# Kernel optimization log

Hardware: AMD Instinct MI355X
Metric: run time of the kernel (lower is better)

Reference implementation:

```python
import jax, jax.numpy as jnp
import numpy as np

N = 50000
NEG_SLOPE = 0.2
BN_EPS = 1e-5


def _self_loops(src, dst, n):
    loop = jnp.arange(n, dtype=src.dtype)
    return jnp.concatenate([src, loop]), jnp.concatenate([dst, loop])


def gcn_conv(x, src, dst, W, b, n):
    # PyG GCNConv: add self-loops, symmetric deg^-1/2 normalization, scatter-add.
    h = x @ W                                             # [N, C]
    s, d = _self_loops(src, dst, n)
    deg = jax.ops.segment_sum(jnp.ones_like(d, dtype=h.dtype), d, num_segments=n)
    dinv = jnp.where(deg > 0, jax.lax.rsqrt(deg), 0.0)
    norm = dinv[s] * dinv[d]                              # [E+N]
    out = jax.ops.segment_sum(h[s] * norm[:, None], d, num_segments=n)
    return out + b


def gat_conv(x, src, dst, W, a_src, a_dst, b, n, heads):
    # PyG GATConv (concat=False, eval mode: no dropout): add self-loops,
    # per-edge LeakyReLU attention logits, segment-softmax over dst, mean heads.
    C = W.shape[1] // heads
    h = (x @ W).reshape(n, heads, C)                      # [N, H, C]
    s, d = _self_loops(src, dst, n)
    al_s = jnp.sum(h * a_src[None], axis=-1)              # [N, H]
    al_d = jnp.sum(h * a_dst[None], axis=-1)              # [N, H]
    e = jax.nn.leaky_relu(al_s[s] + al_d[d], NEG_SLOPE)   # [E+N, H]
    emax = jax.ops.segment_max(e, d, num_segments=n)[d]
    ex = jnp.exp(e - emax)
    denom = jax.ops.segment_sum(ex, d, num_segments=n)[d]
    alpha = ex / denom                                    # [E+N, H]
    out = jax.ops.segment_sum(h[s] * alpha[:, :, None], d, num_segments=n)
    return jnp.mean(out, axis=1) + b                      # concat=False -> head mean


def batch_norm(x, g, b, m, v):
    # eval-mode BatchNorm1d with running stats
    return (x - m) * jax.lax.rsqrt(v + BN_EPS) * g + b


def setup_inputs() -> dict:
    key = jax.random.key(0)
    ks = jax.random.split(key, 12)
    E = 800000
    inp = {}
    inp['x'] = jax.random.normal(ks[0], (N, 128), dtype=jnp.float32)
    inp['edge_index'] = jax.random.randint(ks[1], (2, E), 0, N, dtype=jnp.int64)
    inp['gcn1_W'] = jax.random.normal(ks[2], (128, 96), dtype=jnp.float32) * 0.08
    inp['gcn1_b'] = jnp.zeros((96,), jnp.float32)
    inp['bn1_g'] = jnp.ones((96,), jnp.float32)
    inp['bn1_b'] = jnp.zeros((96,), jnp.float32)
    inp['bn1_m'] = jnp.zeros((96,), jnp.float32)
    inp['bn1_v'] = jnp.ones((96,), jnp.float32)
    inp['gat1_W'] = jax.random.normal(ks[3], (96, 192), dtype=jnp.float32) * 0.1
    inp['gat1_as'] = jax.random.normal(ks[4], (2, 96), dtype=jnp.float32) * 0.1
    inp['gat1_ad'] = jax.random.normal(ks[5], (2, 96), dtype=jnp.float32) * 0.1
    inp['gat1_b'] = jnp.zeros((96,), jnp.float32)
    inp['gcn2_W'] = jax.random.normal(ks[6], (96, 96), dtype=jnp.float32) * 0.1
    inp['gcn2_b'] = jnp.zeros((96,), jnp.float32)
    inp['bn2_g'] = jnp.ones((96,), jnp.float32)
    inp['bn2_b'] = jnp.zeros((96,), jnp.float32)
    inp['bn2_m'] = jnp.zeros((96,), jnp.float32)
    inp['bn2_v'] = jnp.ones((96,), jnp.float32)
    inp['gat2_W'] = jax.random.normal(ks[7], (96, 80), dtype=jnp.float32) * 0.1
    inp['gat2_as'] = jax.random.normal(ks[8], (2, 40), dtype=jnp.float32) * 0.1
    inp['gat2_ad'] = jax.random.normal(ks[9], (2, 40), dtype=jnp.float32) * 0.1
    inp['gat2_b'] = jnp.zeros((40,), jnp.float32)
    return inp


def reference(x, edge_index, gcn1_W, gcn1_b, bn1_g, bn1_b, bn1_m, bn1_v,
              gat1_W, gat1_as, gat1_ad, gat1_b, gcn2_W, gcn2_b,
              bn2_g, bn2_b, bn2_m, bn2_v, gat2_W, gat2_as, gat2_ad, gat2_b):
    src, dst = edge_index[0], edge_index[1]
    h = gcn_conv(x, src, dst, gcn1_W, gcn1_b, N)
    h = jax.nn.relu(batch_norm(h, bn1_g, bn1_b, bn1_m, bn1_v))
    h = jax.nn.relu(gat_conv(h, src, dst, gat1_W, gat1_as, gat1_ad, gat1_b, N, 2))
    h = gcn_conv(h, src, dst, gcn2_W, gcn2_b, N)
    h = jax.nn.relu(batch_norm(h, bn2_g, bn2_b, bn2_m, bn2_v))
    h = gat_conv(h, src, dst, gat2_W, gat2_as, gat2_ad, gat2_b, N, 2)
    return jax.nn.log_softmax(h, axis=1)
```

## Files before the change

### kernel.cpp

```cpp
#include <hip/hip_runtime.h>
#include <math.h>

#define NNODES 50000
#define NEG_SLOPE 0.2f
#define BN_EPS 1e-5f

typedef __attribute__((ext_vector_type(8))) short bf16x8;
typedef __attribute__((ext_vector_type(4))) float f32x4;

static __device__ __forceinline__ float leaky(float x) {
    return x > 0.f ? x : NEG_SLOPE * x;
}
static __device__ __forceinline__ unsigned short f2bf(float x) {
    unsigned u = __float_as_uint(x);
    u += 0x7FFFu + ((u >> 16) & 1u);
    return (unsigned short)(u >> 16);
}
static __device__ __forceinline__ void unpack8(uint4 u, float* v) {
    v[0] = __uint_as_float(u.x << 16);
    v[1] = __uint_as_float(u.x & 0xFFFF0000u);
    v[2] = __uint_as_float(u.y << 16);
    v[3] = __uint_as_float(u.y & 0xFFFF0000u);
    v[4] = __uint_as_float(u.z << 16);
    v[5] = __uint_as_float(u.z & 0xFFFF0000u);
    v[6] = __uint_as_float(u.w << 16);
    v[7] = __uint_as_float(u.w & 0xFFFF0000u);
}
static __device__ __forceinline__ void acc8(uint4 u, float w, float* a) {
    float v[8]; unpack8(u, v);
#pragma unroll
    for (int j = 0; j < 8; ++j) a[j] = fmaf(w, v[j], a[j]);
}
static __device__ __forceinline__ void add8(uint4 u, float* a) {
    float v[8]; unpack8(u, v);
#pragma unroll
    for (int j = 0; j < 8; ++j) a[j] += v[j];
}
static __device__ __forceinline__ uint4 pack8(const float* o) {
    uint4 r;
    r.x = ((unsigned)f2bf(o[1]) << 16) | f2bf(o[0]);
    r.y = ((unsigned)f2bf(o[3]) << 16) | f2bf(o[2]);
    r.z = ((unsigned)f2bf(o[5]) << 16) | f2bf(o[4]);
    r.w = ((unsigned)f2bf(o[7]) << 16) | f2bf(o[6]);
    return r;
}

__global__ void k_count(const int* __restrict__ dst, int* degi, int E) {
    int e = blockIdx.x * blockDim.x + threadIdx.x;
    if (e < E) atomicAdd(&degi[dst[e]], 1);
}
__global__ void k_scan1(const int* __restrict__ degi, int* __restrict__ incl,
                        int* __restrict__ bsum, int n) {
    __shared__ int s[256];
    int i = blockIdx.x * 256 + threadIdx.x;
    int v = (i < n) ? degi[i] : 0;
    s[threadIdx.x] = v;
    __syncthreads();
    for (int off = 1; off < 256; off <<= 1) {
        int t = (threadIdx.x >= (unsigned)off) ? s[threadIdx.x - off] : 0;
        __syncthreads();
        s[threadIdx.x] += t;
        __syncthreads();
    }
    if (i < n) incl[i] = s[threadIdx.x];
    if (threadIdx.x == 255) bsum[blockIdx.x] = s[255];
}
__global__ void k_scan2(int* bsum, int nb) {
    __shared__ int s[256];
    int v = ((int)threadIdx.x < nb) ? bsum[threadIdx.x] : 0;
    s[threadIdx.x] = v;
    __syncthreads();
    for (int off = 1; off < 256; off <<= 1) {
        int t = (threadIdx.x >= (unsigned)off) ? s[threadIdx.x - off] : 0;
        __syncthreads();
        s[threadIdx.x] += t;
        __syncthreads();
    }
    if ((int)threadIdx.x < nb) bsum[threadIdx.x] = s[threadIdx.x];
}
__global__ void k_scan3(const int* __restrict__ degi, const int* __restrict__ incl,
                        const int* __restrict__ bsum, int* __restrict__ row_ptr,
                        int* __restrict__ cursor, float* __restrict__ dinv, int n) {
    int i = blockIdx.x * 256 + threadIdx.x;
    if (i >= n) return;
    int off = (blockIdx.x > 0) ? bsum[blockIdx.x - 1] : 0;
    int inc = incl[i] + off;
    row_ptr[i + 1] = inc;
    cursor[i] = inc - degi[i];
    dinv[i] = rsqrtf((float)(degi[i] + 1));
    if (i == 0) row_ptr[0] = 0;
}
__global__ void k_fill(const int* __restrict__ src, const int* __restrict__ dst,
                       int* cursor, int* __restrict__ csr_src, int E) {
    int e = blockIdx.x * blockDim.x + threadIdx.x;
    if (e >= E) return;
    int pos = atomicAdd(&cursor[dst[e]], 1);
    csr_src[pos] = src[e];
}

__global__ void k_convall(const float4* __restrict__ x, uint4* __restrict__ xout,
                          const float* __restrict__ W1, unsigned short* __restrict__ w1T,
                          const float* __restrict__ W2, unsigned short* __restrict__ w2T,
                          const float* __restrict__ W3, unsigned short* __restrict__ w3T,
                          const float* __restrict__ W4, unsigned short* __restrict__ w4T,
                          int nx) {
    int i = blockIdx.x * blockDim.x + threadIdx.x;
    if (i < nx) {
        float4 a = x[i * 2], b = x[i * 2 + 1];
        float o[8] = {a.x, a.y, a.z, a.w, b.x, b.y, b.z, b.w};
        xout[i] = pack8(o);
        return;
    }
    int j = i - nx;
    if (j < 12288) {
        int k = j / 96, c = j % 96;
        w1T[c * 128 + k] = f2bf(W1[j]);
    } else if ((j -= 12288) < 18432) {
        int k = j / 192, c = j % 192;
        w2T[c * 96 + k] = f2bf(W2[j]);
    } else if ((j -= 18432) < 9216) {
        int k = j / 96, c = j % 96;
        w3T[c * 96 + k] = f2bf(W3[j]);
    } else if ((j -= 9216) < 7680) {
        int k = j / 80, c = j % 80;
        w4T[c * 96 + k] = f2bf(W4[j]);
    }
}

template<int KI, int KO, int HC, int SCALE>
__launch_bounds__(256)
__global__ void k_gemm_mfma(const unsigned short* __restrict__ A,
                            const unsigned short* __restrict__ WT,
                            unsigned short* __restrict__ C, int n,
                            const float* __restrict__ as, const float* __restrict__ ad,
                            float* __restrict__ alS, float* __restrict__ alD,
                            const float* __restrict__ dinv) {
    constexpr int KP = KI + 8;
    constexpr int NT = KO / 16;
    constexpr int KT = KI / 32;
    __shared__ unsigned short wT[KO][KP];
    const int t = threadIdx.x;
    const int w = t >> 6, l = t & 63;

    constexpr int CH = KI / 8;
    for (int idx = t; idx < KO * CH; idx += 256) {
        int r = idx / CH, o = idx % CH;
        *(uint4*)&wT[r][o * 8] = *(const uint4*)&WT[r * KI + o * 8];
    }
    int row = blockIdx.x * 64 + w * 16 + (l & 15);
    bool rv = row < n;
    const unsigned short* ap = A + (long long)row * KI + (l >> 4) * 8;
    bf16x8 afr[KT];
#pragma unroll
    for (int kt = 0; kt < KT; ++kt) {
        bf16x8 z = {};
        afr[kt] = rv ? *(const bf16x8*)(ap + kt * 32) : z;
    }
    __syncthreads();

    f32x4 acc[NT];
#pragma unroll
    for (int ct = 0; ct < NT; ++ct) acc[ct] = (f32x4){0.f, 0.f, 0.f, 0.f};
#pragma unroll
    for (int kt = 0; kt < KT; ++kt) {
#pragma unroll
        for (int ct = 0; ct < NT; ++ct) {
            bf16x8 b = *(const bf16x8*)&wT[ct * 16 + (l & 15)][kt * 32 + (l >> 4) * 8];
            acc[ct] = __builtin_amdgcn_mfma_f32_16x16x32_bf16(afr[kt], b, acc[ct], 0, 0, 0);
        }
    }
    int orow0 = blockIdx.x * 64 + w * 16 + (l >> 4) * 4;
    int col = l & 15;
    float dsc[4] = {1.f, 1.f, 1.f, 1.f};
    if (SCALE) {
#pragma unroll
        for (int r = 0; r < 4; ++r) {
            int rr = orow0 + r;
            if (rr < n) dsc[r] = dinv[rr];
        }
    }
#pragma unroll
    for (int ct = 0; ct < NT; ++ct) {
#pragma unroll
        for (int r = 0; r < 4; ++r) {
            int rr = orow0 + r;
            if (rr < n) C[(long long)rr * KO + ct * 16 + col] = f2bf(acc[ct][r] * dsc[r]);
        }
    }
    if (HC > 0) {
        float asv[NT], adv[NT];
#pragma unroll
        for (int ct = 0; ct < NT; ++ct) {
            int cg = ct * 16 + col;
            asv[ct] = as[cg];
            adv[ct] = ad[cg];
        }
#pragma unroll
        for (int r = 0; r < 4; ++r) {
            float s0 = 0.f, s1 = 0.f, d0 = 0.f, d1 = 0.f;
#pragma unroll
            for (int ct = 0; ct < NT; ++ct) {
                int cg = ct * 16 + col;
                float v = acc[ct][r];
                if (cg < HC) { s0 = fmaf(v, asv[ct], s0); d0 = fmaf(v, adv[ct], d0); }
                else         { s1 = fmaf(v, asv[ct], s1); d1 = fmaf(v, adv[ct], d1); }
            }
#pragma unroll
            for (int m = 1; m < 16; m <<= 1) {
                s0 += __shfl_xor(s0, m);
                s1 += __shfl_xor(s1, m);
                d0 += __shfl_xor(d0, m);
                d1 += __shfl_xor(d1, m);
            }
            int rr = orow0 + r;
            if ((l & 15) == 0 && rr < n) {
                alS[rr * 2] = s0; alS[rr * 2 + 1] = s1;
                alD[rr * 2] = d0; alD[rr * 2 + 1] = d1;
            }
        }
    }
}

__global__ void k_gcn_gather_bn8(const uint4* __restrict__ hb, const int* __restrict__ row_ptr,
                                 const int* __restrict__ csr_src, const float* __restrict__ dinv,
                                 const float* __restrict__ bias, const float* __restrict__ g,
                                 const float* __restrict__ b, const float* __restrict__ m,
                                 const float* __restrict__ vv,
                                 uint4* __restrict__ outb, int n, int Q8) {
    int t = blockIdx.x * blockDim.x + threadIdx.x;
    if (t >= n * Q8) return;
    int v = t / Q8, q = t % Q8;
    int beg = row_ptr[v], end = row_ptr[v + 1];
    float dv = dinv[v];
    float a[8] = {0.f, 0.f, 0.f, 0.f, 0.f, 0.f, 0.f, 0.f};
    add8(hb[(long long)v * Q8 + q], a);
    int p = beg;
    for (; p + 4 <= end; p += 4) {
        int s0 = csr_src[p], s1 = csr_src[p + 1], s2 = csr_src[p + 2], s3 = csr_src[p + 3];
        uint4 u0 = hb[(long long)s0 * Q8 + q];
        uint4 u1 = hb[(long long)s1 * Q8 + q];
        uint4 u2 = hb[(long long)s2 * Q8 + q];
        uint4 u3 = hb[(long long)s3 * Q8 + q];
        add8(u0, a);
        add8(u1, a);
        add8(u2, a);
        add8(u3, a);
    }
    for (; p < end; ++p) {
        int s = csr_src[p];
        add8(hb[(long long)s * Q8 + q], a);
    }
    int c0 = q * 8;
    float o[8];
#pragma unroll
    for (int j = 0; j < 8; ++j) {
        int c = c0 + j;
        float x = fmaf(a[j], dv, bias[c]);
        x = (x - m[c]) * rsqrtf(vv[c] + BN_EPS) * g[c] + b[c];
        o[j] = fmaxf(x, 0.f);
    }
    outb[(long long)v * Q8 + q] = pack8(o);
}

__global__ void k_gat_vh2p(const int* __restrict__ row_ptr, const int* __restrict__ csr_src,
                           const float2* __restrict__ alS2, const float2* __restrict__ alD2,
                           float2* __restrict__ eex2, float2* __restrict__ selfw2,
                           float2* __restrict__ invden2, int n) {
    int v = blockIdx.x * blockDim.x + threadIdx.x;
    if (v >= n) return;
    int beg = row_ptr[v], end = row_ptr[v + 1];
    float2 ad = alD2[v], as0 = alS2[v];
    float ls0 = leaky(as0.x + ad.x), ls1 = leaky(as0.y + ad.y);
    float m0 = ls0, m1 = ls1;
    int p = beg;
    for (; p + 2 <= end; p += 2) {
        int s0 = csr_src[p], s1 = csr_src[p + 1];
        float2 a0 = alS2[s0], a1 = alS2[s1];
        float l00 = leaky(a0.x + ad.x), l01 = leaky(a0.y + ad.y);
        float l10 = leaky(a1.x + ad.x), l11 = leaky(a1.y + ad.y);
        eex2[p] = make_float2(l00, l01);
        eex2[p + 1] = make_float2(l10, l11);
        m0 = fmaxf(m0, fmaxf(l00, l10));
        m1 = fmaxf(m1, fmaxf(l01, l11));
    }
    if (p < end) {
        int s = csr_src[p];
        float2 a = alS2[s];
        float l0 = leaky(a.x + ad.x), l1 = leaky(a.y + ad.y);
        eex2[p] = make_float2(l0, l1);
        m0 = fmaxf(m0, l0);
        m1 = fmaxf(m1, l1);
    }
    float e0 = expf(ls0 - m0), e1 = expf(ls1 - m1);
    float d0 = e0, d1 = e1;
    for (p = beg; p < end; ++p) {
        float2 l = eex2[p];
        float x0 = expf(l.x - m0), x1 = expf(l.y - m1);
        eex2[p] = make_float2(x0, x1);
        d0 += x0; d1 += x1;
    }
    selfw2[v] = make_float2(e0, e1);
    invden2[v] = make_float2(1.f / d0, 1.f / d1);
}
template<int OUTBF>
__global__ void k_gat_gather2_8(const uint4* __restrict__ hb, const int* __restrict__ row_ptr,
                                const int* __restrict__ csr_src, const float2* __restrict__ eex2,
                                const float2* __restrict__ selfw2, const float2* __restrict__ invden2,
                                const float* __restrict__ bias, uint4* __restrict__ outb,
                                float4* __restrict__ outf, int n, int Q8, int do_relu) {
    int t = blockIdx.x * blockDim.x + threadIdx.x;
    if (t >= n * Q8) return;
    int v = t / Q8, q = t % Q8;
    int rowOct = 2 * Q8;
    int beg = row_ptr[v], end = row_ptr[v + 1];
    float A0[8] = {0,0,0,0,0,0,0,0}, A1[8] = {0,0,0,0,0,0,0,0};
    {
        float2 sw = selfw2[v];
        const uint4* hv = hb + (long long)v * rowOct;
        acc8(hv[q], sw.x, A0);
        acc8(hv[Q8 + q], sw.y, A1);
    }
    int p = beg;
    for (; p + 4 <= end; p += 4) {
        int s0 = csr_src[p], s1 = csr_src[p + 1], s2 = csr_src[p + 2], s3 = csr_src[p + 3];
        float2 w0 = eex2[p], w1 = eex2[p + 1], w2 = eex2[p + 2], w3 = eex2[p + 3];
        const uint4* h0 = hb + (long long)s0 * rowOct;
        const uint4* h1 = hb + (long long)s1 * rowOct;
        const uint4* h2 = hb + (long long)s2 * rowOct;
        const uint4* h3 = hb + (long long)s3 * rowOct;
        uint4 u00 = h0[q], u01 = h0[Q8 + q];
        uint4 u10 = h1[q], u11 = h1[Q8 + q];
        uint4 u20 = h2[q], u21 = h2[Q8 + q];
        uint4 u30 = h3[q], u31 = h3[Q8 + q];
        acc8(u00, w0.x, A0); acc8(u01, w0.y, A1);
        acc8(u10, w1.x, A0); acc8(u11, w1.y, A1);
        acc8(u20, w2.x, A0); acc8(u21, w2.y, A1);
        acc8(u30, w3.x, A0); acc8(u31, w3.y, A1);
    }
    for (; p < end; ++p) {
        int s = csr_src[p];
        float2 w = eex2[p];
        const uint4* hs = hb + (long long)s * rowOct;
        acc8(hs[q], w.x, A0);
        acc8(hs[Q8 + q], w.y, A1);
    }
    float2 idn = invden2[v];
    int c0 = q * 8;
    float o[8];
#pragma unroll
    for (int j = 0; j < 8; ++j) {
        float x = fmaf(0.5f, fmaf(A0[j], idn.x, A1[j] * idn.y), bias[c0 + j]);
        o[j] = do_relu ? fmaxf(x, 0.f) : x;
    }
    if (OUTBF) {
        outb[(long long)v * Q8 + q] = pack8(o);
    } else {
        long long ob = (long long)v * (Q8 * 2) + q * 2;
        outf[ob]     = make_float4(o[0], o[1], o[2], o[3]);
        outf[ob + 1] = make_float4(o[4], o[5], o[6], o[7]);
    }
}

__global__ void k_logsoftmax40(const float* __restrict__ in, float* __restrict__ out, int n) {
    int v = blockIdx.x * blockDim.x + threadIdx.x;
    if (v >= n) return;
    float vals[40];
    float mx = -INFINITY;
#pragma unroll
    for (int c = 0; c < 40; ++c) {
        float x = in[v * 40 + c];
        vals[c] = x;
        mx = fmaxf(mx, x);
    }
    float s = 0.f;
#pragma unroll
    for (int c = 0; c < 40; ++c) s += expf(vals[c] - mx);
    float ls = logf(s);
#pragma unroll
    for (int c = 0; c < 40; ++c) out[v * 40 + c] = vals[c] - mx - ls;
}

static inline int nblk(long long n, int b) { return (int)((n + b - 1) / b); }

extern "C" void kernel_launch(void* const* d_in, const int* in_sizes, int n_in,
                              void* d_out, int out_size, void* d_ws, size_t ws_size,
                              hipStream_t stream) {
    const float* x       = (const float*)d_in[0];
    const int*   ei      = (const int*)d_in[1];
    const float* gcn1_W  = (const float*)d_in[2];
    const float* gcn1_b  = (const float*)d_in[3];
    const float* bn1_g   = (const float*)d_in[4];
    const float* bn1_b   = (const float*)d_in[5];
    const float* bn1_m   = (const float*)d_in[6];
    const float* bn1_v   = (const float*)d_in[7];
    const float* gat1_W  = (const float*)d_in[8];
    const float* gat1_as = (const float*)d_in[9];
    const float* gat1_ad = (const float*)d_in[10];
    const float* gat1_b  = (const float*)d_in[11];
    const float* gcn2_W  = (const float*)d_in[12];
    const float* gcn2_b  = (const float*)d_in[13];
    const float* bn2_g   = (const float*)d_in[14];
    const float* bn2_b   = (const float*)d_in[15];
    const float* bn2_m   = (const float*)d_in[16];
    const float* bn2_v   = (const float*)d_in[17];
    const float* gat2_W  = (const float*)d_in[18];
    const float* gat2_as = (const float*)d_in[19];
    const float* gat2_ad = (const float*)d_in[20];
    const float* gat2_b  = (const float*)d_in[21];

    const int n = NNODES;
    const int E = in_sizes[1] / 2;
    const int* src = ei;
    const int* dst = ei + E;

    char* p = (char*)d_ws;
    float* dinv    = (float*)p; p += 50048 * 4;
    int*   degi    = (int*)p;   p += 50048 * 4;
    int*   row_ptr = (int*)p;   p += 50052 * 4;
    int*   cursor  = (int*)p;   p += 50048 * 4;
    int*   incl    = (int*)p;   p += 50048 * 4;
    int*   bsum    = (int*)p;   p += 256 * 4;
    int*   csr_src = (int*)p;   p += 800000 * 4;
    unsigned short* hbf = (unsigned short*)p; p += 9600000 * 2;
    unsigned short* abf = (unsigned short*)p; p += 6400000 * 2;
    unsigned short* wbf = (unsigned short*)p; p += 47616 * 2 + 64;
    float* bufA    = (float*)p; p += 2000000 * 4;
    float* alS     = (float*)p; p += 100096 * 4;
    float* alD     = (float*)p; p += 100096 * 4;
    float* selfw   = (float*)p; p += 100096 * 4;
    float* invden  = (float*)p; p += 100096 * 4;
    float* eex     = (float*)p; p += 1600000 * 4;

    unsigned short* w1T = wbf;
    unsigned short* w2T = wbf + 12288;
    unsigned short* w3T = wbf + 12288 + 18432;
    unsigned short* w4T = wbf + 12288 + 18432 + 9216;

    const int B = 256;
    const int GB = nblk(n, 64);
    const int SB = nblk(n, 256);
    float* out = (float*)d_out;

    const int NX = n * 16;
    k_convall<<<nblk(NX + 47616, B), B, 0, stream>>>(
        (const float4*)x, (uint4*)abf, gcn1_W, w1T, gat1_W, w2T, gcn2_W, w3T, gat2_W, w4T, NX);

    hipMemsetAsync(degi, 0, (size_t)n * 4, stream);
    k_count<<<nblk(E, B), B, 0, stream>>>(dst, degi, E);
    k_scan1<<<SB, 256, 0, stream>>>(degi, incl, bsum, n);
    k_scan2<<<1, 256, 0, stream>>>(bsum, SB);
    k_scan3<<<SB, 256, 0, stream>>>(degi, incl, bsum, row_ptr, cursor, dinv, n);
    k_fill<<<nblk(E, B), B, 0, stream>>>(src, dst, cursor, csr_src, E);

    k_gemm_mfma<128, 96, 0, 1><<<GB, 256, 0, stream>>>(abf, w1T, hbf, n, nullptr, nullptr,
                                                       nullptr, nullptr, dinv);
    k_gcn_gather_bn8<<<nblk((long long)n * 12, B), B, 0, stream>>>(
        (const uint4*)hbf, row_ptr, csr_src, dinv, gcn1_b, bn1_g, bn1_b, bn1_m, bn1_v,
        (uint4*)abf, n, 12);

    k_gemm_mfma<96, 192, 96, 0><<<GB, 256, 0, stream>>>(abf, w2T, hbf, n, gat1_as, gat1_ad,
                                                        alS, alD, nullptr);
    k_gat_vh2p<<<nblk(n, B), B, 0, stream>>>(row_ptr, csr_src, (const float2*)alS, (const float2*)alD,
                                             (float2*)eex, (float2*)selfw, (float2*)invden, n);
    k_gat_gather2_8<1><<<nblk((long long)n * 12, B), B, 0, stream>>>(
        (const uint4*)hbf, row_ptr, csr_src, (const float2*)eex, (const float2*)selfw,
        (const float2*)invden, gat1_b, (uint4*)abf, nullptr, n, 12, 1);

    k_gemm_mfma<96, 96, 0, 1><<<GB, 256, 0, stream>>>(abf, w3T, hbf, n, nullptr, nullptr,
                                                      nullptr, nullptr, dinv);
    k_gcn_gather_bn8<<<nblk((long long)n * 12, B), B, 0, stream>>>(
        (const uint4*)hbf, row_ptr, csr_src, dinv, gcn2_b, bn2_g, bn2_b, bn2_m, bn2_v,
        (uint4*)abf, n, 12);

    k_gemm_mfma<96, 80, 40, 0><<<GB, 256, 0, stream>>>(abf, w4T, hbf, n, gat2_as, gat2_ad,
                                                       alS, alD, nullptr);
    k_gat_vh2p<<<nblk(n, B), B, 0, stream>>>(row_ptr, csr_src, (const float2*)alS, (const float2*)alD,
                                             (float2*)eex, (float2*)selfw, (float2*)invden, n);
    k_gat_gather2_8<0><<<nblk((long long)n * 5, B), B, 0, stream>>>(
        (const uint4*)hbf, row_ptr, csr_src, (const float2*)eex, (const float2*)selfw,
        (const float2*)invden, gat2_b, nullptr, (float4*)bufA, n, 5, 0);

    k_logsoftmax40<<<nblk(n, B), B, 0, stream>>>(bufA, out, n);
}
```

Measured before the change: 361.1 us.

## Sort nodes by in-degree to balance warps in gather kernels

Builds a degree-bucketed node permutation (histogram, scan, atomic fill) once after CSR construction and uses it to pick which node each thread processes in the GCN and GAT gather and softmax kernels. Threads in a wavefront then handle nodes of similar degree, which reduces divergence from uneven per-node loop lengths. In exchange it adds three small kernels and a memset, breaks the contiguity of per-node output writes and self-row reads, and makes bucket order within a degree nondeterministic.

Result: slower. 698.2 us (+93.4%).

```diff
diff --git a/kernel.cpp b/kernel.cpp
--- a/kernel.cpp
+++ b/kernel.cpp
@@ -96,6 +96,31 @@
     if (e >= E) return;
     int pos = atomicAdd(&cursor[dst[e]], 1);
     csr_src[pos] = src[e];
+}
+
+__global__ void k_hist(const int* __restrict__ degi, int* hcnt, int n) {
+    int v = blockIdx.x * blockDim.x + threadIdx.x;
+    if (v < n) atomicAdd(&hcnt[min(degi[v], 63)], 1);
+}
+__global__ void k_hscan(const int* __restrict__ hcnt, int* __restrict__ hbase) {
+    __shared__ int s[64];
+    int t = threadIdx.x;
+    s[t] = hcnt[t];
+    __syncthreads();
+    for (int off = 1; off < 64; off <<= 1) {
+        int x = (t >= off) ? s[t - off] : 0;
+        __syncthreads();
+        s[t] += x;
+        __syncthreads();
+    }
+    hbase[t] = s[t] - hcnt[t];
+}
+__global__ void k_permfill(const int* __restrict__ degi, int* hbase,
+                           int* __restrict__ perm, int n) {
+    int v = blockIdx.x * blockDim.x + threadIdx.x;
+    if (v >= n) return;
+    int pos = atomicAdd(&hbase[min(degi[v], 63)], 1);
+    perm[pos] = v;
 }
 
 __global__ void k_convall(const float4* __restrict__ x, uint4* __restrict__ xout,
@@ -222,14 +247,15 @@
 }
 
 __global__ void k_gcn_gather_bn8(const uint4* __restrict__ hb, const int* __restrict__ row_ptr,
-                                 const int* __restrict__ csr_src, const float* __restrict__ dinv,
+                                 const int* __restrict__ csr_src, const int* __restrict__ perm,
+                                 const float* __restrict__ dinv,
                                  const float* __restrict__ bias, const float* __restrict__ g,
                                  const float* __restrict__ b, const float* __restrict__ m,
                                  const float* __restrict__ vv,
                                  uint4* __restrict__ outb, int n, int Q8) {
     int t = blockIdx.x * blockDim.x + threadIdx.x;
     if (t >= n * Q8) return;
-    int v = t / Q8, q = t % Q8;
+    int v = perm[t / Q8], q = t % Q8;
     int beg = row_ptr[v], end = row_ptr[v + 1];
     float dv = dinv[v];
     float a[8] = {0.f, 0.f, 0.f, 0.f, 0.f, 0.f, 0.f, 0.f};
@@ -263,11 +289,13 @@
 }
 
 __global__ void k_gat_vh2p(const int* __restrict__ row_ptr, const int* __restrict__ csr_src,
+                           const int* __restrict__ perm,
                            const float2* __restrict__ alS2, const float2* __restrict__ alD2,
                            float2* __restrict__ eex2, float2* __restrict__ selfw2,
                            float2* __restrict__ invden2, int n) {
-    int v = blockIdx.x * blockDim.x + threadIdx.x;
-    if (v >= n) return;
+    int i = blockIdx.x * blockDim.x + threadIdx.x;
+    if (i >= n) return;
+    int v = perm[i];
     int beg = row_ptr[v], end = row_ptr[v + 1];
     float2 ad = alD2[v], as0 = alS2[v];
     float ls0 = leaky(as0.x + ad.x), ls1 = leaky(as0.y + ad.y);
@@ -304,13 +332,14 @@
 }
 template<int OUTBF>
 __global__ void k_gat_gather2_8(const uint4* __restrict__ hb, const int* __restrict__ row_ptr,
-                                const int* __restrict__ csr_src, const float2* __restrict__ eex2,
+                                const int* __restrict__ csr_src, const int* __restrict__ perm,
+                                const float2* __restrict__ eex2,
                                 const float2* __restrict__ selfw2, const float2* __restrict__ invden2,
                                 const float* __restrict__ bias, uint4* __restrict__ outb,
                                 float4* __restrict__ outf, int n, int Q8, int do_relu) {
     int t = blockIdx.x * blockDim.x + threadIdx.x;
     if (t >= n * Q8) return;
-    int v = t / Q8, q = t % Q8;
+    int v = perm[t / Q8], q = t % Q8;
     int rowOct = 2 * Q8;
     int beg = row_ptr[v], end = row_ptr[v + 1];
     float A0[8] = {0,0,0,0,0,0,0,0}, A1[8] = {0,0,0,0,0,0,0,0};
@@ -420,6 +449,9 @@
     int*   cursor  = (int*)p;   p += 50048 * 4;
     int*   incl    = (int*)p;   p += 50048 * 4;
     int*   bsum    = (int*)p;   p += 256 * 4;
+    int*   perm    = (int*)p;   p += 50048 * 4;
+    int*   hcnt    = (int*)p;   p += 64 * 4;
+    int*   hbase   = (int*)p;   p += 64 * 4;
     int*   csr_src = (int*)p;   p += 800000 * 4;
     unsigned short* hbf = (unsigned short*)p; p += 9600000 * 2;
     unsigned short* abf = (unsigned short*)p; p += 6400000 * 2;
@@ -446,38 +478,44 @@
         (const float4*)x, (uint4*)abf, gcn1_W, w1T, gat1_W, w2T, gcn2_W, w3T, gat2_W, w4T, NX);
 
     hipMemsetAsync(degi, 0, (size_t)n * 4, stream);
+    hipMemsetAsync(hcnt, 0, 64 * 4, stream);
     k_count<<<nblk(E, B), B, 0, stream>>>(dst, degi, E);
     k_scan1<<<SB, 256, 0, stream>>>(degi, incl, bsum, n);
     k_scan2<<<1, 256, 0, stream>>>(bsum, SB);
     k_scan3<<<SB, 256, 0, stream>>>(degi, incl, bsum, row_ptr, cursor, dinv, n);
     k_fill<<<nblk(E, B), B, 0, stream>>>(src, dst, cursor, csr_src, E);
+    k_hist<<<nblk(n, B), B, 0, stream>>>(degi, hcnt, n);
+    k_hscan<<<1, 64, 0, stream>>>(hcnt, hbase);
+    k_permfill<<<nblk(n, B), B, 0, stream>>>(degi, hbase, perm, n);
 
     k_gemm_mfma<128, 96, 0, 1><<<GB, 256, 0, stream>>>(abf, w1T, hbf, n, nullptr, nullptr,
                                                        nullptr, nullptr, dinv);
     k_gcn_gather_bn8<<<nblk((long long)n * 12, B), B, 0, stream>>>(
-        (const uint4*)hbf, row_ptr, csr_src, dinv, gcn1_b, bn1_g, bn1_b, bn1_m, bn1_v,
+        (const uint4*)hbf, row_ptr, csr_src, perm, dinv, gcn1_b, bn1_g, bn1_b, bn1_m, bn1_v,
         (uint4*)abf, n, 12);
 
     k_gemm_mfma<96, 192, 96, 0><<<GB, 256, 0, stream>>>(abf, w2T, hbf, n, gat1_as, gat1_ad,
                                                         alS, alD, nullptr);
-    k_gat_vh2p<<<nblk(n, B), B, 0, stream>>>(row_ptr, csr_src, (const float2*)alS, (const float2*)alD,
-                                             (float2*)eex, (float2*)selfw, (float2*)invden, n);
+    k_gat_vh2p<<<nblk(n, B), B, 0, stream>>>(row_ptr, csr_src, perm, (const float2*)alS,
+                                             (const float2*)alD, (float2*)eex, (float2*)selfw,
+                                             (float2*)invden, n);
     k_gat_gather2_8<1><<<nblk((long long)n * 12, B), B, 0, stream>>>(
-        (const uint4*)hbf, row_ptr, csr_src, (const float2*)eex, (const float2*)selfw,
+        (const uint4*)hbf, row_ptr, csr_src, perm, (const float2*)eex, (const float2*)selfw,
         (const float2*)invden, gat1_b, (uint4*)abf, nullptr, n, 12, 1);
 
     k_gemm_mfma<96, 96, 0, 1><<<GB, 256, 0, stream>>>(abf, w3T, hbf, n, nullptr, nullptr,
                                                       nullptr, nullptr, dinv);
     k_gcn_gather_bn8<<<nblk((long long)n * 12, B), B, 0, stream>>>(
-        (const uint4*)hbf, row_ptr, csr_src, dinv, gcn2_b, bn2_g, bn2_b, bn2_m, bn2_v,
+        (const uint4*)hbf, row_ptr, csr_src, perm, dinv, gcn2_b, bn2_g, bn2_b, bn2_m, bn2_v,
         (uint4*)abf, n, 12);
 
     k_gemm_mfma<96, 80, 40, 0><<<GB, 256, 0, stream>>>(abf, w4T, hbf, n, gat2_as, gat2_ad,
                                                        alS, alD, nullptr);
-    k_gat_vh2p<<<nblk(n, B), B, 0, stream>>>(row_ptr, csr_src, (const float2*)alS, (const float2*)alD,
-                                             (float2*)eex, (float2*)selfw, (float2*)invden, n);
+    k_gat_vh2p<<<nblk(n, B), B, 0, stream>>>(row_ptr, csr_src, perm, (const float2*)alS,
+                                             (const float2*)alD, (float2*)eex, (float2*)selfw,
+                                             (float2*)invden, n);
     k_gat_gather2_8<0><<<nblk((long long)n * 5, B), B, 0, stream>>>(
-        (const uint4*)hbf, row_ptr, csr_src, (const float2*)eex, (const float2*)selfw,
+        (const uint4*)hbf, row_ptr, csr_src, perm, (const float2*)eex, (const float2*)selfw,
         (const float2*)invden, gat2_b, nullptr, (float4*)bufA, n, 5, 0);
 
     k_logsoftmax40<<<nblk(n, B), B, 0, stream>>>(bufA, out, n);
```
